# Optimization experiments

Measured on AMD Instinct MI355X. Metric: run time of the kernel, lower is better.

Reference implementation:

```python
import jax, jax.numpy as jnp
import numpy as np

# dims: B batch, N seq, D model_dim, R lora rank, C codebooks, K codebook_input_channel, P kv pairs, M per-codebook output
B, N, D, R, C, K, P = 4, 2048, 1024, 8, 64, 16, 64
M = (D * R) // C  # 128


def setup_inputs() -> dict:
    key = jax.random.key(0)
    ks = jax.random.split(key, 7)
    x = jax.random.normal(ks[0], (B, N, D), dtype=jnp.float32)
    W_A = jax.random.normal(ks[1], (C, K, D), dtype=jnp.float32) * (D ** -0.5)
    emb_A = jax.random.uniform(ks[2], (C, P, K), dtype=jnp.float32, minval=-1.5, maxval=1.5)
    vals_A = jax.random.normal(ks[3], (C, P, M), dtype=jnp.float32)
    W_B = jax.random.normal(ks[4], (C, K, D), dtype=jnp.float32) * (D ** -0.5)
    emb_B = jax.random.uniform(ks[5], (C, P, K), dtype=jnp.float32, minval=-1.5, maxval=1.5)
    vals_B = jax.random.normal(ks[6], (C, P, M), dtype=jnp.float32)
    return {"x": x, "W_A": W_A, "emb_A": emb_A, "vals_A": vals_A,
            "W_B": W_B, "emb_B": emb_B, "vals_B": vals_B}


def _discrete_kv(x, W, emb, vals):
    # x: [B,N,D]; W: [C,K,D] (Linear weight per codebook); emb: [C,P,K]; vals: [C,P,M]
    proj = jnp.einsum('bnd,ckd->cbnk', x, W)  # per-codebook linear projection
    # squared euclidean distance to each key (argmin is same as cdist argmin)
    d2 = (jnp.sum(proj * proj, axis=-1, keepdims=True)
          - 2.0 * jnp.einsum('cbnk,cpk->cbnp', proj, emb)
          + jnp.sum(emb * emb, axis=-1)[:, None, None, :])  # [C,B,N,P]
    idx = jnp.argmin(d2, axis=-1)                      # [C,B,N]
    y = jax.vmap(lambda v, i: v[i])(vals, idx)          # [C,B,N,M]
    # concat over codebooks on last dim -> [B,N,C*M], then view as [B,N,R,D]
    return jnp.transpose(y, (1, 2, 0, 3)).reshape(x.shape[0], x.shape[1], R, D)


def reference(x, W_A, emb_A, vals_A, W_B, emb_B, vals_B):
    A = _discrete_kv(x, W_A, emb_A, vals_A)   # [B,N,R,D]
    Bm = _discrete_kv(x, W_B, emb_B, vals_B)  # [B,N,R,D]
    t = jnp.einsum('bnd,bnrd->bnr', x, A)
    return jnp.einsum('bnr,bnrd->bnd', t, Bm)
```

## Files before the change

### kernel.cpp

```cpp
#include <hip/hip_runtime.h>

#define NTOK   8192
#define DMODEL 1024
#define NC     64
#define NK     16
#define NP     64
#define NM     128
#define LCAP   (1 << 18)
#define MARGIN 0.01f

typedef short bf16x8 __attribute__((ext_vector_type(8)));
typedef float f32x4  __attribute__((ext_vector_type(4)));

#define AS1 __attribute__((address_space(1)))
#define AS3 __attribute__((address_space(3)))

__device__ __forceinline__ void glds16(const void* g, void* l) {
    __builtin_amdgcn_global_load_lds((const AS1 void*)g, (AS3 void*)l, 16, 0, 0);
}

__device__ __forceinline__ unsigned f2bf(float f) {
    unsigned u = __builtin_bit_cast(unsigned, f);
    return (u + 0x7FFFu + ((u >> 16) & 1u)) >> 16;
}
__device__ __forceinline__ float bf2f(unsigned s) {
    return __builtin_bit_cast(float, s << 16);
}

__global__ __launch_bounds__(256) void k_split(
    const float* __restrict__ x, const float* __restrict__ W_A, const float* __restrict__ W_B,
    short* __restrict__ xh, short* __restrict__ xl,
    short* __restrict__ whA, short* __restrict__ wlA,
    short* __restrict__ whB, short* __restrict__ wlB)
{
    const int t = blockIdx.x * 256 + threadIdx.x;
    const int NX = 128 * NTOK;
    const int NW = 128 * 1024;

    const float* src;
    short *dh, *dl;
    if (t < NX) {
        const int chunk = t >> 13, tok = t & 8191;
        src = x + (size_t)tok * DMODEL + chunk * 8;
        dh = xh + (size_t)t * 8; dl = xl + (size_t)t * 8;
    } else if (t < NX + NW) {
        const int u = t - NX, chunk = u >> 10, ck = u & 1023;
        src = W_A + (size_t)ck * DMODEL + chunk * 8;
        dh = whA + (size_t)u * 8; dl = wlA + (size_t)u * 8;
    } else {
        const int u = t - NX - NW, chunk = u >> 10, ck = u & 1023;
        src = W_B + (size_t)ck * DMODEL + chunk * 8;
        dh = whB + (size_t)u * 8; dl = wlB + (size_t)u * 8;
    }

    const float4 a = *(const float4*)src;
    const float4 b = *(const float4*)(src + 4);
    const float v[8] = {a.x, a.y, a.z, a.w, b.x, b.y, b.z, b.w};
    unsigned h[8], l[8];
    #pragma unroll
    for (int j = 0; j < 8; ++j) {
        h[j] = f2bf(v[j]);
        l[j] = f2bf(v[j] - bf2f(h[j]));
    }
    *(int4*)dh = make_int4((int)(h[0] | (h[1] << 16)), (int)(h[2] | (h[3] << 16)),
                           (int)(h[4] | (h[5] << 16)), (int)(h[6] | (h[7] << 16)));
    *(int4*)dl = make_int4((int)(l[0] | (l[1] << 16)), (int)(l[2] | (l[3] << 16)),
                           (int)(l[4] | (l[5] << 16)), (int)(l[6] | (l[7] << 16)));
}

__global__ __launch_bounds__(256, 2) void k_mfma_argmin(
    const short* __restrict__ xh, const short* __restrict__ xl,
    const short* __restrict__ whA, const short* __restrict__ wlA,
    const short* __restrict__ whB, const short* __restrict__ wlB,
    const float* __restrict__ emb_A, const float* __restrict__ emb_B,
    int* __restrict__ idxbuf, int* __restrict__ list, int* __restrict__ cnt)
{
    __shared__ __align__(16) float smem[16384];
    short* ls = (short*)smem;
    float* proj = smem;
    float* embS = smem + 8256;
    float* e2S  = smem + 12352;

    const int tid = threadIdx.x;
    const int tb  = blockIdx.x;
    const int ot  = blockIdx.y;
    const int set = ot >> 3;
    const short* __restrict__ wh = set ? whB : whA;
    const short* __restrict__ wl = set ? wlB : wlA;
    const float* __restrict__ Ep = set ? emb_B : emb_A;
    const int cbase = (ot & 7) * 8;

    const int lane = tid & 63;
    const int wid  = tid >> 6;
    const int wr   = wid >> 1;
    const int wc   = wid & 1;
    const int lrow = lane & 15;
    const int lk   = lane >> 4;

    f32x4 acc[4][4];
    #pragma unroll
    for (int m = 0; m < 4; ++m)
        #pragma unroll
        for (int n = 0; n < 4; ++n) acc[m][n] = (f32x4){0.f, 0.f, 0.f, 0.f};

    for (int k0c = 0; k0c < 128; k0c += 8) {
        #pragma unroll
        for (int i = 0; i < 4; ++i) {
            const int u = i * 256 + tid;
            const int ch = u >> 7, r = u & 127;
            const size_t ga = ((size_t)(k0c + ch) * NTOK + tb * 128 + r) * 8;
            glds16(xh + ga, ls + (size_t)u * 8);
            glds16(xl + ga, ls + (size_t)(1024 + u) * 8);
            const size_t gb = ((size_t)(k0c + ch) * 1024 + cbase * 16 + r) * 8;
            glds16(wh + gb, ls + (size_t)(2048 + u) * 8);
            glds16(wl + gb, ls + (size_t)(3072 + u) * 8);
        }
        __syncthreads();
        #pragma unroll
        for (int ks = 0; ks < 2; ++ks) {
            const int cofs = ks * 4 + lk;
            bf16x8 ah[4], al[4], bh[4], bl[4];
            #pragma unroll
            for (int m = 0; m < 4; ++m) {
                const int ua = cofs * 128 + wr * 64 + m * 16 + lrow;
                ah[m] = *(const bf16x8*)(ls + (size_t)ua * 8);
                al[m] = *(const bf16x8*)(ls + (size_t)(1024 + ua) * 8);
                const int ub = cofs * 128 + wc * 64 + m * 16 + lrow;
                bh[m] = *(const bf16x8*)(ls + (size_t)(2048 + ub) * 8);
                bl[m] = *(const bf16x8*)(ls + (size_t)(3072 + ub) * 8);
            }
            #pragma unroll
            for (int m = 0; m < 4; ++m)
                #pragma unroll
                for (int n = 0; n < 4; ++n) {
                    acc[m][n] = __builtin_amdgcn_mfma_f32_16x16x32_bf16(ah[m], bh[n], acc[m][n], 0, 0, 0);
                    acc[m][n] = __builtin_amdgcn_mfma_f32_16x16x32_bf16(ah[m], bl[n], acc[m][n], 0, 0, 0);
                    acc[m][n] = __builtin_amdgcn_mfma_f32_16x16x32_bf16(al[m], bh[n], acc[m][n], 0, 0, 0);
                }
        }
        __syncthreads();
    }

    for (int h = 0; h < 2; ++h) {
        __syncthreads();
        if (wr == h) {
            #pragma unroll
            for (int m = 0; m < 4; ++m)
                #pragma unroll
                for (int n = 0; n < 4; ++n)
                    #pragma unroll
                    for (int r = 0; r < 4; ++r)
                        proj[(m * 16 + lk * 4 + r) * 129 + wc * 64 + n * 16 + lrow] = acc[m][n][r];
        }
        for (int ch = 0; ch < 2; ++ch) {
            __syncthreads();
            {
                const float4* eg = (const float4*)(Ep + (size_t)(cbase + ch * 4) * NP * NK);
                float4* es = (float4*)embS;
                #pragma unroll
                for (int i = 0; i < 4; ++i) es[tid + 256 * i] = eg[tid + 256 * i];
            }
            __syncthreads();
            {
                const float* e = embS + tid * 16;
                float s = 0.f;
                #pragma unroll
                for (int k = 0; k < 16; ++k) s = fmaf(e[k], e[k], s);
                e2S[tid] = s;
            }
            __syncthreads();
            {
                const int cl = tid >> 6, lt = tid & 63;
                float pr[16];
                const float* pp = proj + lt * 129 + (ch * 4 + cl) * 16;
                #pragma unroll
                for (int k = 0; k < 16; ++k) pr[k] = pp[k];
                const float* eb = embS + cl * 1024;
                const float* e2 = e2S + cl * 64;
                float best = 1e30f, second = 1e30f;
                int bp = 0;
                for (int p = 0; p < 64; ++p) {
                    const float* e = eb + p * 16;
                    float s = 0.f;
                    #pragma unroll
                    for (int k = 0; k < 16; ++k) s = fmaf(pr[k], e[k], s);
                    const float g = fmaf(-2.f, s, e2[p]);
                    if (g < best) { second = best; best = g; bp = p; }
                    else if (g < second) { second = g; }
                }
                const int c = cbase + ch * 4 + cl;
                const int gtok = tb * 128 + h * 64 + lt;
                idxbuf[(set * NC + c) * NTOK + gtok] = bp;
                if (second - best < MARGIN) {
                    const int slot = atomicAdd(cnt, 1);
                    if (slot < LCAP) list[slot] = (set << 19) | (c << 13) | gtok;
                }
            }
        }
    }
}

__global__ __launch_bounds__(256) void k_refine(
    const float* __restrict__ x,
    const float* __restrict__ W_A, const float* __restrict__ W_B,
    const float* __restrict__ emb_A, const float* __restrict__ emb_B,
    const int* __restrict__ list, const int* __restrict__ cnt,
    int* __restrict__ idxbuf)
{
    int n = *cnt;
    if (n > LCAP) n = LCAP;
    const int lane = threadIdx.x & 63;
    const int wave = (int)((blockIdx.x * blockDim.x + threadIdx.x) >> 6);
    const int nw   = (int)((gridDim.x * blockDim.x) >> 6);

    for (int i = wave; i < n; i += nw) {
        const int code = list[i];
        const int tok = code & 8191;
        const int c   = (code >> 13) & 63;
        const int set = (code >> 19) & 1;
        const float* __restrict__ Wp = set ? W_B : W_A;
        const float* __restrict__ Ep = set ? emb_B : emb_A;

        double pk[16];
        #pragma unroll
        for (int k = 0; k < 16; ++k) pk[k] = 0.0;
        for (int dd = 0; dd < 16; ++dd) {
            const int d = dd * 64 + lane;
            const double xv = (double)x[(size_t)tok * DMODEL + d];
            #pragma unroll
            for (int k = 0; k < 16; ++k)
                pk[k] = fma(xv, (double)Wp[(size_t)(c * 16 + k) * DMODEL + d], pk[k]);
        }
        #pragma unroll
        for (int k = 0; k < 16; ++k) {
            #pragma unroll
            for (int off = 32; off; off >>= 1)
                pk[k] += __shfl_xor(pk[k], off, 64);
        }
        double d2 = 0.0;
        #pragma unroll
        for (int k = 0; k < 16; ++k) {
            const double t = pk[k] - (double)Ep[(size_t)(c * NP + lane) * NK + k];
            d2 = fma(t, t, d2);
        }
        int bp = lane;
        double bv = d2;
        #pragma unroll
        for (int off = 32; off; off >>= 1) {
            const double ov = __shfl_xor(bv, off, 64);
            const int    op = __shfl_xor(bp, off, 64);
            if (ov < bv || (ov == bv && op < bp)) { bv = ov; bp = op; }
        }
        if (lane == 0) idxbuf[(set * NC + c) * NTOK + tok] = bp;
    }
}

__global__ __launch_bounds__(256) void k_combine(
    const float* __restrict__ x,
    const float* __restrict__ vals_A, const float* __restrict__ vals_B,
    const int* __restrict__ idxbuf, float* __restrict__ out)
{
    __shared__ float xsh[1032];
    __shared__ float part[256];
    __shared__ float tsh[8];
    __shared__ int sIA[64];
    __shared__ int sIB[64];

    const int tid = threadIdx.x;
    const int tok = blockIdx.x;

    if (tid < 64) {
        sIA[tid] = idxbuf[tid * NTOK + tok];
        sIB[tid] = idxbuf[(NC + tid) * NTOK + tok];
    }
    {
        const float4 v = *(const float4*)(x + (size_t)tok * DMODEL + tid * 4);
        const int base = tid * 4 + (tid >> 5);
        xsh[base + 0] = v.x;
        xsh[base + 1] = v.y;
        xsh[base + 2] = v.z;
        xsh[base + 3] = v.w;
    }
    __syncthreads();
    {
        const int c = tid & 63, mseg = tid >> 6;
        const int ia = sIA[c];
        const float4* va = (const float4*)(vals_A + (size_t)(c * NP + ia) * NM + mseg * 32);
        const float* xb = xsh + (c & 7) * 129 + mseg * 32;
        float s = 0.f;
        #pragma unroll
        for (int i = 0; i < 8; ++i) {
            const float4 v = va[i];
            s = fmaf(v.x, xb[i * 4 + 0], s);
            s = fmaf(v.y, xb[i * 4 + 1], s);
            s = fmaf(v.z, xb[i * 4 + 2], s);
            s = fmaf(v.w, xb[i * 4 + 3], s);
        }
        part[tid] = s;
    }
    __syncthreads();
    if (tid < 8) {
        float s = 0.f;
        #pragma unroll
        for (int m = 0; m < 4; ++m)
            #pragma unroll
            for (int j = 0; j < 8; ++j)
                s += part[m * 64 + tid * 8 + j];
        tsh[tid] = s;
    }
    __syncthreads();
    {
        const int d0 = tid * 4, dblk = tid >> 5, dm = d0 & 127;
        float o0 = 0.f, o1 = 0.f, o2 = 0.f, o3 = 0.f;
        #pragma unroll
        for (int r = 0; r < 8; ++r) {
            const int cb = 8 * r + dblk;
            const int ib = sIB[cb];
            const float4 v = *(const float4*)(vals_B + (size_t)(cb * NP + ib) * NM + dm);
            const float tv = tsh[r];
            o0 = fmaf(tv, v.x, o0);
            o1 = fmaf(tv, v.y, o1);
            o2 = fmaf(tv, v.z, o2);
            o3 = fmaf(tv, v.w, o3);
        }
        *(float4*)(out + (size_t)tok * DMODEL + d0) = make_float4(o0, o1, o2, o3);
    }
}

extern "C" void kernel_launch(void* const* d_in, const int* in_sizes, int n_in,
                              void* d_out, int out_size, void* d_ws, size_t ws_size,
                              hipStream_t stream)
{
    const float* x      = (const float*)d_in[0];
    const float* W_A    = (const float*)d_in[1];
    const float* emb_A  = (const float*)d_in[2];
    const float* vals_A = (const float*)d_in[3];
    const float* W_B    = (const float*)d_in[4];
    const float* emb_B  = (const float*)d_in[5];
    const float* vals_B = (const float*)d_in[6];
    float* out = (float*)d_out;

    char* w = (char*)d_ws;
    int*   cnt    = (int*)w;
    int*   list   = (int*)(w + 16);
    int*   idxbuf = (int*)(w + 16 + sizeof(int) * (size_t)LCAP);
    size_t off = 16 + sizeof(int) * (size_t)LCAP + sizeof(int) * (size_t)(2 * NC * NTOK);
    short* xh  = (short*)(w + off); off += (size_t)NTOK * DMODEL * 2;
    short* xl  = (short*)(w + off); off += (size_t)NTOK * DMODEL * 2;
    short* whA = (short*)(w + off); off += (size_t)1024 * DMODEL * 2;
    short* wlA = (short*)(w + off); off += (size_t)1024 * DMODEL * 2;
    short* whB = (short*)(w + off); off += (size_t)1024 * DMODEL * 2;
    short* wlB = (short*)(w + off);

    hipMemsetAsync(cnt, 0, sizeof(int), stream);
    k_split<<<5120, 256, 0, stream>>>(x, W_A, W_B, xh, xl, whA, wlA, whB, wlB);
    k_mfma_argmin<<<dim3(64, 16), 256, 0, stream>>>(xh, xl, whA, wlA, whB, wlB,
                                                    emb_A, emb_B, idxbuf, list, cnt);
    k_refine<<<1024, 256, 0, stream>>>(x, W_A, W_B, emb_A, emb_B, list, cnt, idxbuf);
    k_combine<<<NTOK, 256, 0, stream>>>(x, vals_A, vals_B, idxbuf, out);
}
```

Before: 250.6 us.

## Use single fp16 MFMA with wider refine margin and double-buffered LDS staging

Replaces the three-pass split-bf16 projection GEMM with a single fp16 MFMA pass, dropping the low-part x and W buffers and their conversion writes. To compensate for the lower precision, the near-tie margin that sends tokens to the exact fp32 refine kernel grows from 0.01 to 0.045. The k-loop now double-buffers its global-to-LDS loads so the next tile loads while the current one is computed. It also pads the proj and embedding LDS layouts and vectorizes the distance loop with float4 reads. The cost is more refine-list entries and reliance on fp16 range and precision being adequate for these inputs.

```diff
diff --git a/kernel.cpp b/kernel.cpp
--- a/kernel.cpp
+++ b/kernel.cpp
@@ -7,10 +7,10 @@
 #define NP     64
 #define NM     128
 #define LCAP   (1 << 18)
-#define MARGIN 0.01f
-
-typedef short bf16x8 __attribute__((ext_vector_type(8)));
-typedef float f32x4  __attribute__((ext_vector_type(4)));
+#define MARGIN 0.045f
+
+typedef _Float16 f16x8 __attribute__((ext_vector_type(8)));
+typedef float    f32x4 __attribute__((ext_vector_type(4)));
 
 #define AS1 __attribute__((address_space(1)))
 #define AS3 __attribute__((address_space(3)))
@@ -19,74 +19,57 @@
     __builtin_amdgcn_global_load_lds((const AS1 void*)g, (AS3 void*)l, 16, 0, 0);
 }
 
-__device__ __forceinline__ unsigned f2bf(float f) {
-    unsigned u = __builtin_bit_cast(unsigned, f);
-    return (u + 0x7FFFu + ((u >> 16) & 1u)) >> 16;
-}
-__device__ __forceinline__ float bf2f(unsigned s) {
-    return __builtin_bit_cast(float, s << 16);
-}
-
 __global__ __launch_bounds__(256) void k_split(
     const float* __restrict__ x, const float* __restrict__ W_A, const float* __restrict__ W_B,
-    short* __restrict__ xh, short* __restrict__ xl,
-    short* __restrict__ whA, short* __restrict__ wlA,
-    short* __restrict__ whB, short* __restrict__ wlB)
+    short* __restrict__ xh, short* __restrict__ whA, short* __restrict__ whB)
 {
     const int t = blockIdx.x * 256 + threadIdx.x;
     const int NX = 128 * NTOK;
     const int NW = 128 * 1024;
 
     const float* src;
-    short *dh, *dl;
+    short* dh;
     if (t < NX) {
         const int chunk = t >> 13, tok = t & 8191;
         src = x + (size_t)tok * DMODEL + chunk * 8;
-        dh = xh + (size_t)t * 8; dl = xl + (size_t)t * 8;
+        dh = xh + (size_t)t * 8;
     } else if (t < NX + NW) {
         const int u = t - NX, chunk = u >> 10, ck = u & 1023;
         src = W_A + (size_t)ck * DMODEL + chunk * 8;
-        dh = whA + (size_t)u * 8; dl = wlA + (size_t)u * 8;
+        dh = whA + (size_t)u * 8;
     } else {
         const int u = t - NX - NW, chunk = u >> 10, ck = u & 1023;
         src = W_B + (size_t)ck * DMODEL + chunk * 8;
-        dh = whB + (size_t)u * 8; dl = wlB + (size_t)u * 8;
+        dh = whB + (size_t)u * 8;
     }
 
     const float4 a = *(const float4*)src;
     const float4 b = *(const float4*)(src + 4);
     const float v[8] = {a.x, a.y, a.z, a.w, b.x, b.y, b.z, b.w};
-    unsigned h[8], l[8];
+    unsigned h[8];
     #pragma unroll
-    for (int j = 0; j < 8; ++j) {
-        h[j] = f2bf(v[j]);
-        l[j] = f2bf(v[j] - bf2f(h[j]));
-    }
+    for (int j = 0; j < 8; ++j)
+        h[j] = (unsigned)__builtin_bit_cast(unsigned short, (_Float16)v[j]);
     *(int4*)dh = make_int4((int)(h[0] | (h[1] << 16)), (int)(h[2] | (h[3] << 16)),
                            (int)(h[4] | (h[5] << 16)), (int)(h[6] | (h[7] << 16)));
-    *(int4*)dl = make_int4((int)(l[0] | (l[1] << 16)), (int)(l[2] | (l[3] << 16)),
-                           (int)(l[4] | (l[5] << 16)), (int)(l[6] | (l[7] << 16)));
 }
 
 __global__ __launch_bounds__(256, 2) void k_mfma_argmin(
-    const short* __restrict__ xh, const short* __restrict__ xl,
-    const short* __restrict__ whA, const short* __restrict__ wlA,
-    const short* __restrict__ whB, const short* __restrict__ wlB,
+    const short* __restrict__ xh, const short* __restrict__ whA, const short* __restrict__ whB,
     const float* __restrict__ emb_A, const float* __restrict__ emb_B,
     int* __restrict__ idxbuf, int* __restrict__ list, int* __restrict__ cnt)
 {
     __shared__ __align__(16) float smem[16384];
     short* ls = (short*)smem;
     float* proj = smem;
-    float* embS = smem + 8256;
-    float* e2S  = smem + 12352;
+    float* embS = smem + 8448;
+    float* e2S  = smem + 12576;
 
     const int tid = threadIdx.x;
     const int tb  = blockIdx.x;
     const int ot  = blockIdx.y;
     const int set = ot >> 3;
     const short* __restrict__ wh = set ? whB : whA;
-    const short* __restrict__ wl = set ? wlB : wlA;
     const float* __restrict__ Ep = set ? emb_B : emb_A;
     const int cbase = (ot & 7) * 8;
 
@@ -103,43 +86,44 @@
         #pragma unroll
         for (int n = 0; n < 4; ++n) acc[m][n] = (f32x4){0.f, 0.f, 0.f, 0.f};
 
-    for (int k0c = 0; k0c < 128; k0c += 8) {
-        #pragma unroll
-        for (int i = 0; i < 4; ++i) {
-            const int u = i * 256 + tid;
-            const int ch = u >> 7, r = u & 127;
-            const size_t ga = ((size_t)(k0c + ch) * NTOK + tb * 128 + r) * 8;
-            glds16(xh + ga, ls + (size_t)u * 8);
-            glds16(xl + ga, ls + (size_t)(1024 + u) * 8);
-            const size_t gb = ((size_t)(k0c + ch) * 1024 + cbase * 16 + r) * 8;
-            glds16(wh + gb, ls + (size_t)(2048 + u) * 8);
-            glds16(wl + gb, ls + (size_t)(3072 + u) * 8);
-        }
-        __syncthreads();
+    #define STAGE(buf, k0c)                                                             \
+        do {                                                                            \
+            _Pragma("unroll")                                                           \
+            for (int i_ = 0; i_ < 4; ++i_) {                                            \
+                const int u_ = i_ * 256 + tid;                                          \
+                const int ch_ = u_ >> 7, r_ = u_ & 127;                                 \
+                glds16(xh + ((size_t)((k0c) + ch_) * NTOK + tb * 128 + r_) * 8,         \
+                       ls + (size_t)((buf) * 2048 + u_) * 8);                           \
+                glds16(wh + ((size_t)((k0c) + ch_) * 1024 + cbase * 16 + r_) * 8,       \
+                       ls + (size_t)((buf) * 2048 + 1024 + u_) * 8);                    \
+            }                                                                           \
+        } while (0)
+
+    STAGE(0, 0);
+    __syncthreads();
+    int cur = 0;
+    for (int step = 0; step < 16; ++step) {
+        if (step < 15) STAGE(cur ^ 1, (step + 1) * 8);
+        const int cb = cur * 2048;
         #pragma unroll
         for (int ks = 0; ks < 2; ++ks) {
             const int cofs = ks * 4 + lk;
-            bf16x8 ah[4], al[4], bh[4], bl[4];
+            f16x8 a[4], b[4];
             #pragma unroll
             for (int m = 0; m < 4; ++m) {
-                const int ua = cofs * 128 + wr * 64 + m * 16 + lrow;
-                ah[m] = *(const bf16x8*)(ls + (size_t)ua * 8);
-                al[m] = *(const bf16x8*)(ls + (size_t)(1024 + ua) * 8);
-                const int ub = cofs * 128 + wc * 64 + m * 16 + lrow;
-                bh[m] = *(const bf16x8*)(ls + (size_t)(2048 + ub) * 8);
-                bl[m] = *(const bf16x8*)(ls + (size_t)(3072 + ub) * 8);
+                a[m] = *(const f16x8*)(ls + (size_t)(cb + cofs * 128 + wr * 64 + m * 16 + lrow) * 8);
+                b[m] = *(const f16x8*)(ls + (size_t)(cb + 1024 + cofs * 128 + wc * 64 + m * 16 + lrow) * 8);
             }
             #pragma unroll
             for (int m = 0; m < 4; ++m)
                 #pragma unroll
-                for (int n = 0; n < 4; ++n) {
-                    acc[m][n] = __builtin_amdgcn_mfma_f32_16x16x32_bf16(ah[m], bh[n], acc[m][n], 0, 0, 0);
-                    acc[m][n] = __builtin_amdgcn_mfma_f32_16x16x32_bf16(ah[m], bl[n], acc[m][n], 0, 0, 0);
-                    acc[m][n] = __builtin_amdgcn_mfma_f32_16x16x32_bf16(al[m], bh[n], acc[m][n], 0, 0, 0);
-                }
+                for (int n = 0; n < 4; ++n)
+                    acc[m][n] = __builtin_amdgcn_mfma_f32_16x16x32_f16(a[m], b[n], acc[m][n], 0, 0, 0);
         }
         __syncthreads();
-    }
+        cur ^= 1;
+    }
+    #undef STAGE
 
     for (int h = 0; h < 2; ++h) {
         __syncthreads();
@@ -150,19 +134,22 @@
                 for (int n = 0; n < 4; ++n)
                     #pragma unroll
                     for (int r = 0; r < 4; ++r)
-                        proj[(m * 16 + lk * 4 + r) * 129 + wc * 64 + n * 16 + lrow] = acc[m][n][r];
+                        proj[(m * 16 + lk * 4 + r) * 132 + wc * 64 + n * 16 + lrow] = acc[m][n][r];
         }
         for (int ch = 0; ch < 2; ++ch) {
             __syncthreads();
             {
                 const float4* eg = (const float4*)(Ep + (size_t)(cbase + ch * 4) * NP * NK);
-                float4* es = (float4*)embS;
-                #pragma unroll
-                for (int i = 0; i < 4; ++i) es[tid + 256 * i] = eg[tid + 256 * i];
+                #pragma unroll
+                for (int i = 0; i < 4; ++i) {
+                    const int idx = tid + 256 * i;
+                    const int cb4 = idx >> 8, win = idx & 255;
+                    ((float4*)(embS + cb4 * 1032))[win] = eg[idx];
+                }
             }
             __syncthreads();
             {
-                const float* e = embS + tid * 16;
+                const float* e = embS + (tid >> 6) * 1032 + (tid & 63) * 16;
                 float s = 0.f;
                 #pragma unroll
                 for (int k = 0; k < 16; ++k) s = fmaf(e[k], e[k], s);
@@ -172,18 +159,29 @@
             {
                 const int cl = tid >> 6, lt = tid & 63;
                 float pr[16];
-                const float* pp = proj + lt * 129 + (ch * 4 + cl) * 16;
-                #pragma unroll
-                for (int k = 0; k < 16; ++k) pr[k] = pp[k];
-                const float* eb = embS + cl * 1024;
+                const float4* pp = (const float4*)(proj + lt * 132 + (ch * 4 + cl) * 16);
+                #pragma unroll
+                for (int q = 0; q < 4; ++q) {
+                    const float4 v = pp[q];
+                    pr[q * 4 + 0] = v.x; pr[q * 4 + 1] = v.y;
+                    pr[q * 4 + 2] = v.z; pr[q * 4 + 3] = v.w;
+                }
+                const float4* eb4 = (const float4*)(embS + cl * 1032);
                 const float* e2 = e2S + cl * 64;
                 float best = 1e30f, second = 1e30f;
                 int bp = 0;
                 for (int p = 0; p < 64; ++p) {
-                    const float* e = eb + p * 16;
+                    const float4 e0 = eb4[p * 4 + 0], e1 = eb4[p * 4 + 1];
+                    const float4 e2v = eb4[p * 4 + 2], e3 = eb4[p * 4 + 3];
                     float s = 0.f;
-                    #pragma unroll
-                    for (int k = 0; k < 16; ++k) s = fmaf(pr[k], e[k], s);
+                    s = fmaf(pr[0], e0.x, s);  s = fmaf(pr[1], e0.y, s);
+                    s = fmaf(pr[2], e0.z, s);  s = fmaf(pr[3], e0.w, s);
+                    s = fmaf(pr[4], e1.x, s);  s = fmaf(pr[5], e1.y, s);
+                    s = fmaf(pr[6], e1.z, s);  s = fmaf(pr[7], e1.w, s);
+                    s = fmaf(pr[8], e2v.x, s); s = fmaf(pr[9], e2v.y, s);
+                    s = fmaf(pr[10], e2v.z, s); s = fmaf(pr[11], e2v.w, s);
+                    s = fmaf(pr[12], e3.x, s); s = fmaf(pr[13], e3.y, s);
+                    s = fmaf(pr[14], e3.z, s); s = fmaf(pr[15], e3.w, s);
                     const float g = fmaf(-2.f, s, e2[p]);
                     if (g < best) { second = best; best = g; bp = p; }
                     else if (g < second) { second = g; }
@@ -346,15 +344,12 @@
     int*   idxbuf = (int*)(w + 16 + sizeof(int) * (size_t)LCAP);
     size_t off = 16 + sizeof(int) * (size_t)LCAP + sizeof(int) * (size_t)(2 * NC * NTOK);
     short* xh  = (short*)(w + off); off += (size_t)NTOK * DMODEL * 2;
-    short* xl  = (short*)(w + off); off += (size_t)NTOK * DMODEL * 2;
     short* whA = (short*)(w + off); off += (size_t)1024 * DMODEL * 2;
-    short* wlA = (short*)(w + off); off += (size_t)1024 * DMODEL * 2;
-    short* whB = (short*)(w + off); off += (size_t)1024 * DMODEL * 2;
-    short* wlB = (short*)(w + off);
+    short* whB = (short*)(w + off);
 
     hipMemsetAsync(cnt, 0, sizeof(int), stream);
-    k_split<<<5120, 256, 0, stream>>>(x, W_A, W_B, xh, xl, whA, wlA, whB, wlB);
-    k_mfma_argmin<<<dim3(64, 16), 256, 0, stream>>>(xh, xl, whA, wlA, whB, wlB,
+    k_split<<<5120, 256, 0, stream>>>(x, W_A, W_B, xh, whA, whB);
+    k_mfma_argmin<<<dim3(64, 16), 256, 0, stream>>>(xh, whA, whB,
                                                     emb_A, emb_B, idxbuf, list, cnt);
     k_refine<<<1024, 256, 0, stream>>>(x, W_A, W_B, emb_A, emb_B, list, cnt, idxbuf);
     k_combine<<<NTOK, 256, 0, stream>>>(x, vals_A, vals_B, idxbuf, out);
```

Measured after the change: 326.8 us. 1.3x slower.
